# Kernel optimization log

Hardware: AMD Instinct MI355X
Metric: run time of the kernel (lower is better)

## Reference

```python
import jax, jax.numpy as jnp
import numpy as np

N = 30000
E = 300000
DIN, DH, DOUT, L = 256, 128, 64, 6


def setup_inputs() -> dict:
    key = jax.random.key(0)
    ks = jax.random.split(key, 8)
    feats = jax.random.normal(ks[0], (N, DIN), dtype=jnp.float32)
    src = jax.random.randint(ks[1], (E,), 0, N, dtype=jnp.int32)
    dst = jax.random.randint(ks[2], (E,), 0, N, dtype=jnp.int32)
    W0 = jax.random.normal(ks[3], (DIN, DH), dtype=jnp.float32) * 0.05
    b0 = jnp.zeros((DH,), dtype=jnp.float32)
    Wh = jax.random.normal(ks[4], (L, DH, DH), dtype=jnp.float32) * 0.05
    bh = jnp.zeros((L, DH), dtype=jnp.float32)
    Wout = jax.random.normal(ks[5], (DH * (L + 1), DOUT), dtype=jnp.float32) * 0.05
    bout = jnp.zeros((DOUT,), dtype=jnp.float32)
    return {"feats": feats, "src": src, "dst": dst, "W0": W0, "b0": b0,
            "Wh": Wh, "bh": bh, "Wout": Wout, "bout": bout}


def _graph_conv(x, W, b, src, dst, inv_sqrt_out, inv_sqrt_in):
    # DGL GraphConv, norm='both': D_out^{-1/2} -> sum over edges -> D_in^{-1/2} -> XW+b -> relu
    x = x * inv_sqrt_out[:, None]
    m = jax.ops.segment_sum(x[src], dst, num_segments=N)  # [N, d]
    m = m * inv_sqrt_in[:, None]
    return jax.nn.relu(m @ W + b)


def reference(feats, src, dst, W0, b0, Wh, bh, Wout, bout):
    ones = jnp.ones((E,), dtype=jnp.float32)
    out_deg = jax.ops.segment_sum(ones, src, num_segments=N)
    in_deg = jax.ops.segment_sum(ones, dst, num_segments=N)
    inv_sqrt_out = jax.lax.rsqrt(jnp.clip(out_deg, 1.0))
    inv_sqrt_in = jax.lax.rsqrt(jnp.clip(in_deg, 1.0))

    h = _graph_conv(feats, W0, b0, src, dst, inv_sqrt_out, inv_sqrt_in)
    reps = [h]
    for i in range(L):
        h = _graph_conv(h, Wh[i], bh[i], src, dst, inv_sqrt_out, inv_sqrt_in)
        reps.append(h)
    jk = jnp.concatenate(reps, axis=-1)  # [N, DH*(L+1)]
    # update_all(copy_u, sum): un-normalized neighborhood sum
    h = jax.ops.segment_sum(jk[src], dst, num_segments=N)
    return h @ Wout + bout
```

## Files before the change

kernel.cpp:

```cpp
#include <hip/hip_runtime.h>

#define NN 30000
#define NE 300000
#define D_IN 256
#define D_H 128
#define D_OUT 64
#define NL 6
#define NB ((NN + 255) / 256)
#define NTILE (NN / 16)
#define G0TILE ((NN + 31) / 32)

typedef unsigned short ushort_t;
typedef unsigned int uint_t;
typedef __attribute__((ext_vector_type(8))) short sh8;
typedef __attribute__((ext_vector_type(4))) float f4;

static __device__ __forceinline__ ushort_t f2bf(float f) {
    uint_t u = __float_as_uint(f);
    u = (u + 0x7FFFu + ((u >> 16) & 1u)) >> 16;
    return (ushort_t)u;
}

__global__ void degree_kernel(const int* __restrict__ src, const int* __restrict__ dst,
                              int* __restrict__ outdeg, int* __restrict__ indeg) {
    int e = blockIdx.x * blockDim.x + threadIdx.x;
    if (e < NE) {
        atomicAdd(&outdeg[src[e]], 1);
        atomicAdd(&indeg[dst[e]], 1);
    }
}

__global__ void rsqrt_kernel(const int* __restrict__ deg, float* __restrict__ inv, int n) {
    int i = blockIdx.x * blockDim.x + threadIdx.x;
    if (i < n) {
        float d = (float)deg[i];
        inv[i] = rsqrtf(d < 1.0f ? 1.0f : d);
    }
}

__global__ __launch_bounds__(256) void bsum_kernel(const int* __restrict__ deg,
                                                   int* __restrict__ bsum) {
    __shared__ int wsum[4];
    int t = threadIdx.x, lane = t & 63, w = t >> 6;
    int i = blockIdx.x * 256 + t;
    int v = (i < NN) ? deg[i] : 0;
#pragma unroll
    for (int off = 32; off; off >>= 1) v += __shfl_down(v, off, 64);
    if (lane == 0) wsum[w] = v;
    __syncthreads();
    if (t == 0) bsum[blockIdx.x] = wsum[0] + wsum[1] + wsum[2] + wsum[3];
}

__global__ __launch_bounds__(128) void boffs_kernel(const int* __restrict__ bsum,
                                                    int* __restrict__ boffs,
                                                    int* __restrict__ row_ptr) {
    __shared__ int wtot[2];
    int t = threadIdx.x, lane = t & 63, w = t >> 6;
    int v = (t < NB) ? bsum[t] : 0;
    int s = v;
#pragma unroll
    for (int off = 1; off < 64; off <<= 1) {
        int x = __shfl_up(s, off, 64);
        if (lane >= off) s += x;
    }
    if (lane == 63) wtot[w] = s;
    __syncthreads();
    int add = (w == 1) ? wtot[0] : 0;
    if (t < NB) boffs[t] = add + s - v;
    if (t == 0) row_ptr[NN] = NE;
}

__global__ __launch_bounds__(256) void rowptr_kernel(const int* __restrict__ deg,
                                                     const int* __restrict__ boffs,
                                                     int* __restrict__ row_ptr) {
    __shared__ int wsum[4];
    int t = threadIdx.x, lane = t & 63, w = t >> 6;
    int i = blockIdx.x * 256 + t;
    int v = (i < NN) ? deg[i] : 0;
    int s = v;
#pragma unroll
    for (int off = 1; off < 64; off <<= 1) {
        int x = __shfl_up(s, off, 64);
        if (lane >= off) s += x;
    }
    if (lane == 63) wsum[w] = s;
    __syncthreads();
    int woff = 0;
#pragma unroll
    for (int k = 0; k < 4; k++)
        if (k < w) woff += wsum[k];
    if (i < NN) row_ptr[i] = boffs[blockIdx.x] + woff + s - v;
}

__global__ void fill_kernel(const int* __restrict__ src, const int* __restrict__ dst,
                            const int* __restrict__ row_ptr, int* __restrict__ cursor,
                            int* __restrict__ col) {
    int e = blockIdx.x * blockDim.x + threadIdx.x;
    if (e < NE) {
        int d = dst[e];
        int pos = atomicAdd(&cursor[d], 1);
        col[row_ptr[d] + pos] = src[e];
    }
}

__global__ void packw_kernel(const float* __restrict__ W0,
                             const float* __restrict__ Wh,
                             const float* __restrict__ Wout,
                             ushort_t* __restrict__ W0p,
                             ushort_t* __restrict__ Whp,
                             ushort_t* __restrict__ Woutp) {
    int g = blockIdx.x * blockDim.x + threadIdx.x;
    int frag = g >> 6;
    int lane = g & 63;
    if (frag >= 368) return;
    const float* srcw;
    ushort_t* dstp;
    int fl, KF, M;
    if (frag < 64) {
        fl = frag; KF = 8; M = 128;
        srcw = W0;
        dstp = W0p;
    } else if (frag < 64 + 192) {
        int f2 = frag - 64;
        int l = f2 / 32; fl = f2 % 32; KF = 4; M = 128;
        srcw = Wh + (size_t)l * D_H * D_H;
        dstp = Whp + (size_t)l * 32 * 512;
    } else {
        int f2 = frag - 256;
        int l = f2 / 16; fl = f2 % 16; KF = 4; M = 64;
        srcw = Wout + (size_t)l * D_H * D_OUT;
        dstp = Woutp + (size_t)l * 16 * 512;
    }
    int ct = fl / KF;
    int kt = fl % KF;
    int krow = kt * 32 + (lane >> 4) * 8;
    int cidx = ct * 16 + (lane & 15);
    ushort_t tmp[8];
#pragma unroll
    for (int j = 0; j < 8; j++)
        tmp[j] = f2bf(srcw[(size_t)(krow + j) * M + cidx]);
    uint4 o;
    o.x = (uint_t)tmp[0] | ((uint_t)tmp[1] << 16);
    o.y = (uint_t)tmp[2] | ((uint_t)tmp[3] << 16);
    o.z = (uint_t)tmp[4] | ((uint_t)tmp[5] << 16);
    o.w = (uint_t)tmp[6] | ((uint_t)tmp[7] << 16);
    *(uint4*)(dstp + (size_t)fl * 512 + lane * 8) = o;
}

__global__ __launch_bounds__(256) void gemm0_kernel(
    const float* __restrict__ X,
    const ushort_t* __restrict__ W1p,
    const float* __restrict__ scale,
    ushort_t* __restrict__ Tb)
{
    constexpr int KF = 8;
    const int lane = threadIdx.x & 63;
    const int w = threadIdx.x >> 6;
    const int rg = w >> 1;
    const int cgrp = w & 1;
    const int row0 = blockIdx.x * 32 + rg * 16;

    int arow = row0 + (lane & 15);
    if (arow >= NN) arow = NN - 1;
    const float* xr = X + (size_t)arow * D_IN + ((lane >> 4) * 8);
    sh8 a[KF];
#pragma unroll
    for (int kt = 0; kt < KF; kt++) {
        float4 lo = *(const float4*)(xr + kt * 32);
        float4 hi = *(const float4*)(xr + kt * 32 + 4);
        sh8 t;
        t[0] = (short)f2bf(lo.x); t[1] = (short)f2bf(lo.y);
        t[2] = (short)f2bf(lo.z); t[3] = (short)f2bf(lo.w);
        t[4] = (short)f2bf(hi.x); t[5] = (short)f2bf(hi.y);
        t[6] = (short)f2bf(hi.z); t[7] = (short)f2bf(hi.w);
        a[kt] = t;
    }

    const int crow0 = row0 + (lane >> 4) * 4;
    float s[4];
#pragma unroll
    for (int r = 0; r < 4; r++) {
        int rw = crow0 + r;
        s[r] = scale[rw < NN ? rw : NN - 1];
    }
#pragma unroll
    for (int i = 0; i < 4; i++) {
        int ct = cgrp * 4 + i;
        f4 acc = {0.f, 0.f, 0.f, 0.f};
        const ushort_t* wp = W1p + ((size_t)(ct * KF) << 9) + lane * 8;
#pragma unroll
        for (int kt = 0; kt < KF; kt++)
            acc = __builtin_amdgcn_mfma_f32_16x16x32_bf16(
                a[kt], *(const sh8*)(wp + ((size_t)kt << 9)), acc, 0, 0, 0);
        int colb = ct * 16 + (lane & 15);
#pragma unroll
        for (int r = 0; r < 4; r++) {
            int rw = crow0 + r;
            if (rw < NN)
                Tb[(size_t)rw * 128 + colb] = f2bf(acc[r] * s[r]);
        }
    }
}

static __device__ __forceinline__ void acc8(float* acc, uint4 u) {
    uint_t wv[4] = {u.x, u.y, u.z, u.w};
#pragma unroll
    for (int i = 0; i < 4; i++) {
        acc[2 * i]     += __uint_as_float(wv[i] << 16);
        acc[2 * i + 1] += __uint_as_float(wv[i] & 0xFFFF0000u);
    }
}

template <bool HAS_T, bool HAS_P>
__global__ __launch_bounds__(256, 5) void fused4_kernel(
    const ushort_t* __restrict__ Tin,
    const int* __restrict__ row_ptr,
    const int* __restrict__ col,
    const float* __restrict__ inv_in,
    const float* __restrict__ bias,
    const ushort_t* __restrict__ W1p,
    const ushort_t* __restrict__ W2p,
    const float* __restrict__ inv_out,
    ushort_t* __restrict__ Tout,
    float* __restrict__ P)
{
    __shared__ float part[4 * 32 * 64];
    const int tid = threadIdx.x;
    const int lane = tid & 63;
    const int w = tid >> 6;
    const int row0 = blockIdx.x * 16;
    const int r = row0 + (lane & 15);
    const int beg = row_ptr[r];
    const int end = row_ptr[r + 1];
    const int cb = (lane >> 4) * 8;
    const int cq = (lane >> 4) * 4;

    const int cnt = end - beg;
    const int j0 = beg + ((cnt * w) >> 2);
    const int j1 = beg + ((cnt * (w + 1)) >> 2);

    float acc[4][8];
#pragma unroll
    for (int kt = 0; kt < 4; kt++)
#pragma unroll
        for (int i = 0; i < 8; i++) acc[kt][i] = 0.f;

    const uint_t* T32 = (const uint_t*)Tin;
    int j = j0;
    for (; j + 1 < j1; j += 2) {
        int c0 = col[j], c1 = col[j + 1];
        const uint_t* p0 = T32 + (size_t)c0 * 64 + cq;
        const uint_t* p1 = T32 + (size_t)c1 * 64 + cq;
        uint4 u00 = *(const uint4*)(p0);
        uint4 u01 = *(const uint4*)(p0 + 16);
        uint4 u02 = *(const uint4*)(p0 + 32);
        uint4 u03 = *(const uint4*)(p0 + 48);
        uint4 u10 = *(const uint4*)(p1);
        uint4 u11 = *(const uint4*)(p1 + 16);
        uint4 u12 = *(const uint4*)(p1 + 32);
        uint4 u13 = *(const uint4*)(p1 + 48);
        acc8(acc[0], u00); acc8(acc[0], u10);
        acc8(acc[1], u01); acc8(acc[1], u11);
        acc8(acc[2], u02); acc8(acc[2], u12);
        acc8(acc[3], u03); acc8(acc[3], u13);
    }
    if (j < j1) {
        int c0 = col[j];
        const uint_t* p0 = T32 + (size_t)c0 * 64 + cq;
        acc8(acc[0], *(const uint4*)(p0));
        acc8(acc[1], *(const uint4*)(p0 + 16));
        acc8(acc[2], *(const uint4*)(p0 + 32));
        acc8(acc[3], *(const uint4*)(p0 + 48));
    }

#pragma unroll
    for (int kt = 0; kt < 4; kt++)
#pragma unroll
        for (int i = 0; i < 8; i++)
            part[(w * 32 + kt * 8 + i) * 64 + lane] = acc[kt][i];
    __syncthreads();

#pragma unroll
    for (int ow = 1; ow < 4; ow++) {
        int w2 = (w + ow) & 3;
#pragma unroll
        for (int kt = 0; kt < 4; kt++)
#pragma unroll
            for (int i = 0; i < 8; i++)
                acc[kt][i] += part[(w2 * 32 + kt * 8 + i) * 64 + lane];
    }

    const float s = inv_in[r];
    sh8 a[4];
#pragma unroll
    for (int kt = 0; kt < 4; kt++) {
        float4 b0 = *(const float4*)(bias + kt * 32 + cb);
        float4 b1 = *(const float4*)(bias + kt * 32 + cb + 4);
        float bb[8] = {b0.x, b0.y, b0.z, b0.w, b1.x, b1.y, b1.z, b1.w};
        sh8 t;
#pragma unroll
        for (int i = 0; i < 8; i++) {
            float h = fmaxf(fmaf(acc[kt][i], s, bb[i]), 0.f);
            t[i] = (short)f2bf(h);
        }
        a[kt] = t;
    }

    const int crow0 = row0 + (lane >> 4) * 4;

    if (HAS_T) {
        float sc[4];
#pragma unroll
        for (int rr = 0; rr < 4; rr++)
            sc[rr] = inv_out[crow0 + rr];
#pragma unroll
        for (int u = 0; u < 3; u++) {
            int unit = w * 3 + u;
            if (unit < 8) {
                int ct = unit;
                f4 accT = {0.f, 0.f, 0.f, 0.f};
                const ushort_t* wp = W1p + ((size_t)(ct * 4) << 9) + lane * 8;
#pragma unroll
                for (int kt = 0; kt < 4; kt++)
                    accT = __builtin_amdgcn_mfma_f32_16x16x32_bf16(
                        a[kt], *(const sh8*)(wp + ((size_t)kt << 9)), accT, 0, 0, 0);
                int colb = ct * 16 + (lane & 15);
#pragma unroll
                for (int rr = 0; rr < 4; rr++)
                    Tout[(size_t)(crow0 + rr) * 128 + colb] = f2bf(accT[rr] * sc[rr]);
            } else {
                int ct = unit - 8;
                f4 accP = {0.f, 0.f, 0.f, 0.f};
                const ushort_t* wp = W2p + ((size_t)(ct * 4) << 9) + lane * 8;
#pragma unroll
                for (int kt = 0; kt < 4; kt++)
                    accP = __builtin_amdgcn_mfma_f32_16x16x32_bf16(
                        a[kt], *(const sh8*)(wp + ((size_t)kt << 9)), accP, 0, 0, 0);
                int colb = ct * 16 + (lane & 15);
#pragma unroll
                for (int rr = 0; rr < 4; rr++)
                    P[(size_t)(crow0 + rr) * 64 + colb] += accP[rr];
            }
        }
    } else if (HAS_P) {
        int ct = w;
        f4 accP = {0.f, 0.f, 0.f, 0.f};
        const ushort_t* wp = W2p + ((size_t)(ct * 4) << 9) + lane * 8;
#pragma unroll
        for (int kt = 0; kt < 4; kt++)
            accP = __builtin_amdgcn_mfma_f32_16x16x32_bf16(
                a[kt], *(const sh8*)(wp + ((size_t)kt << 9)), accP, 0, 0, 0);
        int colb = ct * 16 + (lane & 15);
#pragma unroll
        for (int rr = 0; rr < 4; rr++)
            P[(size_t)(crow0 + rr) * 64 + colb] += accP[rr];
    }
}

__global__ __launch_bounds__(256) void gather_f32_kernel(
    const float* __restrict__ P,
    const int* __restrict__ row_ptr,
    const int* __restrict__ col,
    const float* __restrict__ bias,
    float* __restrict__ Y) {
    int idx = blockIdx.x * blockDim.x + threadIdx.x;
    int node = idx >> 4;
    int q = idx & 15;
    if (node >= NN) return;
    int beg = row_ptr[node];
    int end = row_ptr[node + 1];
    float4 acc = make_float4(0.f, 0.f, 0.f, 0.f);
    int j = beg;
    for (; j + 3 < end; j += 4) {
        int c0 = col[j], c1 = col[j + 1], c2 = col[j + 2], c3 = col[j + 3];
        float4 v0 = *(const float4*)(P + (size_t)c0 * 64 + q * 4);
        float4 v1 = *(const float4*)(P + (size_t)c1 * 64 + q * 4);
        float4 v2 = *(const float4*)(P + (size_t)c2 * 64 + q * 4);
        float4 v3 = *(const float4*)(P + (size_t)c3 * 64 + q * 4);
        acc.x += (v0.x + v1.x) + (v2.x + v3.x);
        acc.y += (v0.y + v1.y) + (v2.y + v3.y);
        acc.z += (v0.z + v1.z) + (v2.z + v3.z);
        acc.w += (v0.w + v1.w) + (v2.w + v3.w);
    }
    for (; j < end; j++) {
        int c0 = col[j];
        float4 v0 = *(const float4*)(P + (size_t)c0 * 64 + q * 4);
        acc.x += v0.x; acc.y += v0.y; acc.z += v0.z; acc.w += v0.w;
    }
    float4 b = *(const float4*)(bias + q * 4);
    acc.x += b.x; acc.y += b.y; acc.z += b.z; acc.w += b.w;
    *(float4*)(Y + (size_t)node * 64 + q * 4) = acc;
}

extern "C" void kernel_launch(void* const* d_in, const int* in_sizes, int n_in,
                              void* d_out, int out_size, void* d_ws, size_t ws_size,
                              hipStream_t stream) {
    const float* feats = (const float*)d_in[0];
    const int*   src   = (const int*)d_in[1];
    const int*   dst   = (const int*)d_in[2];
    const float* W0    = (const float*)d_in[3];
    const float* b0    = (const float*)d_in[4];
    const float* Wh    = (const float*)d_in[5];
    const float* bh    = (const float*)d_in[6];
    const float* Wout  = (const float*)d_in[7];
    const float* bout  = (const float*)d_in[8];
    float* out = (float*)d_out;

    float* ws      = (float*)d_ws;
    float* inv_out = ws;
    float* inv_in  = ws + NN;
    float* p       = ws + 2 * NN;
    ushort_t* tb   = (ushort_t*)(p + (size_t)NN * 64);
    ushort_t* ha   = tb + (size_t)NN * 128;
    ushort_t* hb   = ha + (size_t)NN * 128;
    ushort_t* fb   = hb + (size_t)NN * 128;
    ushort_t* w0p  = fb + (size_t)NN * 256;
    ushort_t* whp  = w0p + 64 * 512;
    ushort_t* wop  = whp + 192 * 512;
    int* ibase     = (int*)(wop + 112 * 512);
    int* outdeg_i  = ibase;
    int* indeg_i   = ibase + NN;
    int* cursor    = ibase + 2 * NN;
    int* row_ptr   = ibase + 3 * NN;
    int* col       = ibase + 4 * NN + 1;
    int* bsum      = (int*)hb;
    int* boffs     = bsum + NB + 8;

    const int B = 256;
    const int gather_blocks = (NN * 16 + B - 1) / B;

    (void)hipMemsetAsync(ibase, 0, 3 * NN * sizeof(int), stream);
    (void)hipMemsetAsync(p, 0, (size_t)NN * D_OUT * sizeof(float), stream);
    degree_kernel<<<(NE + B - 1) / B, B, 0, stream>>>(src, dst, outdeg_i, indeg_i);
    rsqrt_kernel<<<(2 * NN + B - 1) / B, B, 0, stream>>>(outdeg_i, inv_out, 2 * NN);
    bsum_kernel<<<NB, 256, 0, stream>>>(indeg_i, bsum);
    boffs_kernel<<<1, 128, 0, stream>>>(bsum, boffs, row_ptr);
    rowptr_kernel<<<NB, 256, 0, stream>>>(indeg_i, boffs, row_ptr);
    fill_kernel<<<(NE + B - 1) / B, B, 0, stream>>>(src, dst, row_ptr, cursor, col);
    packw_kernel<<<(368 * 64 + B - 1) / B, B, 0, stream>>>(W0, Wh, Wout, w0p, whp, wop);

    gemm0_kernel<<<G0TILE, 256, 0, stream>>>(feats, w0p, inv_out, tb);

    const ushort_t* tcur = tb;
    ushort_t* tnext = ha;
    for (int l = 0; l < NL; l++) {
        const float* bias_l = (l == 0) ? b0 : bh + (size_t)(l - 1) * D_H;
        fused4_kernel<true, true><<<NTILE, 256, 0, stream>>>(
            tcur, row_ptr, col, inv_in, bias_l,
            whp + (size_t)l * 32 * 512, wop + (size_t)l * 16 * 512,
            inv_out, tnext, p);
        const ushort_t* t = tcur; tcur = tnext; tnext = (ushort_t*)t;
    }
    fused4_kernel<false, true><<<NTILE, 256, 0, stream>>>(
        tcur, row_ptr, col, inv_in, bh + (size_t)(NL - 1) * D_H,
        nullptr, wop + (size_t)NL * 16 * 512, nullptr, nullptr, p);

    gather_f32_kernel<<<gather_blocks, B, 0, stream>>>(p, row_ptr, col, bout, out);
}
```

Measured before the change: 327.1 us.

## Sort nodes by in-degree via histogram permutation to balance gather tiles

Builds a counting-sort permutation of nodes keyed by in-degree (capped at 63) using histogram, scan and scatter kernels. The fused layer kernels and the final gather then process rows in that order, so each 16-row tile has similar neighbor counts and lanes in a wavefront do not wait on one high-degree row. The cost is three extra small kernels, an indirection load per row, and scattered rather than contiguous output row writes to T and P.

```diff
diff --git a/kernel.cpp b/kernel.cpp
--- a/kernel.cpp
+++ b/kernel.cpp
@@ -100,6 +100,38 @@
         int d = dst[e];
         int pos = atomicAdd(&cursor[d], 1);
         col[row_ptr[d] + pos] = src[e];
+    }
+}
+
+__global__ void hist_kernel(const int* __restrict__ indeg, int* __restrict__ hist) {
+    int i = blockIdx.x * blockDim.x + threadIdx.x;
+    if (i < NN) {
+        int b = indeg[i]; if (b > 63) b = 63;
+        atomicAdd(&hist[b], 1);
+    }
+}
+
+__global__ __launch_bounds__(64) void hscan_kernel(const int* __restrict__ hist,
+                                                   int* __restrict__ hoff) {
+    int lane = threadIdx.x;
+    int v = hist[lane];
+    int s = v;
+#pragma unroll
+    for (int off = 1; off < 64; off <<= 1) {
+        int t = __shfl_up(s, off, 64);
+        if (lane >= off) s += t;
+    }
+    hoff[lane] = s - v;
+}
+
+__global__ void permscatter_kernel(const int* __restrict__ indeg,
+                                   int* __restrict__ hoff,
+                                   int* __restrict__ perm) {
+    int i = blockIdx.x * blockDim.x + threadIdx.x;
+    if (i < NN) {
+        int b = indeg[i]; if (b > 63) b = 63;
+        int pos = atomicAdd(&hoff[b], 1);
+        perm[pos] = i;
     }
 }
 
@@ -216,6 +248,7 @@
     const ushort_t* __restrict__ Tin,
     const int* __restrict__ row_ptr,
     const int* __restrict__ col,
+    const int* __restrict__ perm,
     const float* __restrict__ inv_in,
     const float* __restrict__ bias,
     const ushort_t* __restrict__ W1p,
@@ -229,7 +262,7 @@
     const int lane = tid & 63;
     const int w = tid >> 6;
     const int row0 = blockIdx.x * 16;
-    const int r = row0 + (lane & 15);
+    const int r = perm[row0 + (lane & 15)];
     const int beg = row_ptr[r];
     const int end = row_ptr[r + 1];
     const int cb = (lane >> 4) * 8;
@@ -307,12 +340,16 @@
     }
 
     const int crow0 = row0 + (lane >> 4) * 4;
+    int prow[4];
+#pragma unroll
+    for (int rr = 0; rr < 4; rr++)
+        prow[rr] = perm[crow0 + rr];
 
     if (HAS_T) {
         float sc[4];
 #pragma unroll
         for (int rr = 0; rr < 4; rr++)
-            sc[rr] = inv_out[crow0 + rr];
+            sc[rr] = inv_out[prow[rr]];
 #pragma unroll
         for (int u = 0; u < 3; u++) {
             int unit = w * 3 + u;
@@ -327,7 +364,7 @@
                 int colb = ct * 16 + (lane & 15);
 #pragma unroll
                 for (int rr = 0; rr < 4; rr++)
-                    Tout[(size_t)(crow0 + rr) * 128 + colb] = f2bf(accT[rr] * sc[rr]);
+                    Tout[(size_t)prow[rr] * 128 + colb] = f2bf(accT[rr] * sc[rr]);
             } else {
                 int ct = unit - 8;
                 f4 accP = {0.f, 0.f, 0.f, 0.f};
@@ -339,7 +376,7 @@
                 int colb = ct * 16 + (lane & 15);
 #pragma unroll
                 for (int rr = 0; rr < 4; rr++)
-                    P[(size_t)(crow0 + rr) * 64 + colb] += accP[rr];
+                    P[(size_t)prow[rr] * 64 + colb] += accP[rr];
             }
         }
     } else if (HAS_P) {
@@ -353,7 +390,7 @@
         int colb = ct * 16 + (lane & 15);
 #pragma unroll
         for (int rr = 0; rr < 4; rr++)
-            P[(size_t)(crow0 + rr) * 64 + colb] += accP[rr];
+            P[(size_t)prow[rr] * 64 + colb] += accP[rr];
     }
 }
 
@@ -361,12 +398,14 @@
     const float* __restrict__ P,
     const int* __restrict__ row_ptr,
     const int* __restrict__ col,
+    const int* __restrict__ perm,
     const float* __restrict__ bias,
     float* __restrict__ Y) {
     int idx = blockIdx.x * blockDim.x + threadIdx.x;
-    int node = idx >> 4;
+    int slot = idx >> 4;
     int q = idx & 15;
-    if (node >= NN) return;
+    if (slot >= NN) return;
+    int node = perm[slot];
     int beg = row_ptr[node];
     int end = row_ptr[node + 1];
     float4 acc = make_float4(0.f, 0.f, 0.f, 0.f);
@@ -421,15 +460,18 @@
     int* outdeg_i  = ibase;
     int* indeg_i   = ibase + NN;
     int* cursor    = ibase + 2 * NN;
-    int* row_ptr   = ibase + 3 * NN;
-    int* col       = ibase + 4 * NN + 1;
+    int* hist      = ibase + 3 * NN;
+    int* row_ptr   = ibase + 3 * NN + 64;
+    int* col       = ibase + 4 * NN + 65;
+    int* perm      = ibase + 4 * NN + 65 + NE;
+    int* hoff      = perm + NN;
     int* bsum      = (int*)hb;
     int* boffs     = bsum + NB + 8;
 
     const int B = 256;
     const int gather_blocks = (NN * 16 + B - 1) / B;
 
-    (void)hipMemsetAsync(ibase, 0, 3 * NN * sizeof(int), stream);
+    (void)hipMemsetAsync(ibase, 0, (3 * NN + 64) * sizeof(int), stream);
     (void)hipMemsetAsync(p, 0, (size_t)NN * D_OUT * sizeof(float), stream);
     degree_kernel<<<(NE + B - 1) / B, B, 0, stream>>>(src, dst, outdeg_i, indeg_i);
     rsqrt_kernel<<<(2 * NN + B - 1) / B, B, 0, stream>>>(outdeg_i, inv_out, 2 * NN);
@@ -437,6 +479,9 @@
     boffs_kernel<<<1, 128, 0, stream>>>(bsum, boffs, row_ptr);
     rowptr_kernel<<<NB, 256, 0, stream>>>(indeg_i, boffs, row_ptr);
     fill_kernel<<<(NE + B - 1) / B, B, 0, stream>>>(src, dst, row_ptr, cursor, col);
+    hist_kernel<<<NB, 256, 0, stream>>>(indeg_i, hist);
+    hscan_kernel<<<1, 64, 0, stream>>>(hist, hoff);
+    permscatter_kernel<<<NB, 256, 0, stream>>>(indeg_i, hoff, perm);
     packw_kernel<<<(368 * 64 + B - 1) / B, B, 0, stream>>>(W0, Wh, Wout, w0p, whp, wop);
 
     gemm0_kernel<<<G0TILE, 256, 0, stream>>>(feats, w0p, inv_out, tb);
@@ -446,14 +491,14 @@
     for (int l = 0; l < NL; l++) {
         const float* bias_l = (l == 0) ? b0 : bh + (size_t)(l - 1) * D_H;
         fused4_kernel<true, true><<<NTILE, 256, 0, stream>>>(
-            tcur, row_ptr, col, inv_in, bias_l,
+            tcur, row_ptr, col, perm, inv_in, bias_l,
             whp + (size_t)l * 32 * 512, wop + (size_t)l * 16 * 512,
             inv_out, tnext, p);
         const ushort_t* t = tcur; tcur = tnext; tnext = (ushort_t*)t;
     }
     fused4_kernel<false, true><<<NTILE, 256, 0, stream>>>(
-        tcur, row_ptr, col, inv_in, bh + (size_t)(NL - 1) * D_H,
+        tcur, row_ptr, col, perm, inv_in, bh + (size_t)(NL - 1) * D_H,
         nullptr, wop + (size_t)NL * 16 * 512, nullptr, nullptr, p);
 
-    gather_f32_kernel<<<gather_blocks, B, 0, stream>>>(p, row_ptr, col, bout, out);
-}
+    gather_f32_kernel<<<gather_blocks, B, 0, stream>>>(p, row_ptr, col, perm, bout, out);
+}
```

After: 562.9 us. 1.72x slower.
